# Kernel optimization log

Measured on AMD Instinct MI355X. Metric: run time of the kernel, lower is better.

## Reference

```python
import jax, jax.numpy as jnp
import numpy as np
import math

B, S, D, H = 4, 2048, 1024, 16
HD = D // H  # 64

def setup_inputs() -> dict:
    key = jax.random.key(0)
    ks = jax.random.split(key, 4)
    x = jax.random.normal(ks[0], (B, S, D), dtype=jnp.float32)
    # causal mask, True = attend (precomputed as in the original usage)
    mask = jnp.tril(jnp.ones((S, S), dtype=bool))[None, None, :, :]
    c_attn_w = jax.random.normal(ks[1], (D, 3 * D), dtype=jnp.float32) * 0.02
    c_attn_b = jnp.zeros((3 * D,), dtype=jnp.float32)
    c_proj_w = jax.random.normal(ks[2], (D, D), dtype=jnp.float32) * 0.02
    c_proj_b = jnp.zeros((D,), dtype=jnp.float32)
    return {"x": x, "mask": mask, "c_attn_w": c_attn_w, "c_attn_b": c_attn_b,
            "c_proj_w": c_proj_w, "c_proj_b": c_proj_b}

def reference(x, mask, c_attn_w, c_attn_b, c_proj_w, c_proj_b):
    b, s, d = x.shape
    # c_attn: Conv1D acts as Linear with transposed weight convention
    qkv = x @ c_attn_w + c_attn_b                      # [B,S,3D]
    q, k, v = jnp.split(qkv, 3, axis=-1)
    q = q.reshape(b, s, H, HD).transpose(0, 2, 1, 3)   # [B,H,S,hd]
    k = k.reshape(b, s, H, HD).transpose(0, 2, 1, 3)   # [B,H,S,hd]
    v = v.reshape(b, s, H, HD).transpose(0, 2, 1, 3)   # [B,H,S,hd]
    # scores, scale by sqrt(head_dim) (done unconditionally in _attn)
    w = jnp.einsum('bhqd,bhkd->bhqk', q, k) / math.sqrt(HD)
    # masked_fill_(1 - mask, -10000.0)
    w = jnp.where(mask, w, jnp.float32(-10000.0))
    w = jax.nn.softmax(w, axis=-1)                     # attn_dropout p=0
    a = jnp.einsum('bhqk,bhkd->bhqd', w, v)            # [B,H,S,hd]
    a = a.transpose(0, 2, 1, 3).reshape(b, s, d)       # merge heads
    out = a @ c_proj_w + c_proj_b                      # resid_dropout p=0
    return out
```

## Files before the change

kernel.cpp:

```cpp
#include <hip/hip_runtime.h>

#define SEQ  2048
#define DIM  1024
#define NH   16
#define HD   64
#define NB   4

typedef __bf16 bf16_t;
typedef bf16_t bf16x8 __attribute__((ext_vector_type(8)));
typedef bf16_t bf16x4 __attribute__((ext_vector_type(4)));
typedef float  floatx4 __attribute__((ext_vector_type(4)));

#define MFMA16(a, b, c) __builtin_amdgcn_mfma_f32_16x16x32_bf16((a), (b), (c), 0, 0, 0)

__device__ __forceinline__ void gl_lds16(const bf16_t* g, bf16_t* l) {
    __builtin_amdgcn_global_load_lds(
        (const __attribute__((address_space(1))) void*)g,
        (__attribute__((address_space(3))) void*)l,
        16, 0, 0);
}

__global__ __launch_bounds__(256) void prep(
    const float* __restrict__ x, bf16_t* __restrict__ xb,
    const float* __restrict__ wqkv, bf16_t* __restrict__ wqkvT,
    const float* __restrict__ wproj, bf16_t* __restrict__ wprojT) {
    const int bid = blockIdx.x, tid = threadIdx.x;
    if (bid < 8192) {
        const int i = (bid * 256 + tid) * 4;
        const float4 v = *(const float4*)(x + i);
        xb[i + 0] = (bf16_t)v.x;
        xb[i + 1] = (bf16_t)v.y;
        xb[i + 2] = (bf16_t)v.z;
        xb[i + 3] = (bf16_t)v.w;
        return;
    }
    __shared__ bf16_t t[32][33];
    const float* in;
    bf16_t* out;
    int R, C, bx, by;
    if (bid < 8192 + 3072) {
        const int idx = bid - 8192;
        in = wqkv; out = wqkvT; R = 1024; C = 3072;
        bx = idx % 96; by = idx / 96;
    } else {
        const int idx = bid - 11264;
        in = wproj; out = wprojT; R = 1024; C = 1024;
        bx = idx & 31; by = idx >> 5;
    }
    const int c0 = bx * 32, r0 = by * 32;
    const int tx = tid & 31, ty = tid >> 5;
#pragma unroll
    for (int i = 0; i < 32; i += 8)
        t[ty + i][tx] = (bf16_t)in[(r0 + ty + i) * C + c0 + tx];
    __syncthreads();
#pragma unroll
    for (int i = 0; i < 32; i += 8)
        out[(c0 + ty + i) * R + r0 + tx] = t[tx][ty + i];
}

template <int MODE>
__global__ __launch_bounds__(256, 2) void gemm128(
    const bf16_t* __restrict__ A, const bf16_t* __restrict__ Bt,
    const float* __restrict__ bias, int K,
    bf16_t* __restrict__ Qo, bf16_t* __restrict__ Ko, bf16_t* __restrict__ Vo,
    float* __restrict__ Co) {
    __shared__ __align__(16) bf16_t smem[MODE == 0 ? 128 * 136 : 128 * 128];
    bf16_t* Al = smem;
    bf16_t* Bl = smem + 128 * 64;

    const int tid = threadIdx.x;
    const int m0 = blockIdx.y * 128, n0 = blockIdx.x * 128;
    const int w = tid >> 6, lane = tid & 63;
    const int l15 = lane & 15, quad = lane >> 4;
    const int wm = (w & 1) * 64, wn = (w >> 1) * 64;

    floatx4 acc[4][4] = {};

    const int g_st = ((tid & 7) - (tid >> 3)) & 7;
    const bf16_t* aptr = A + (m0 + (tid >> 3)) * K + g_st * 8;
    const bf16_t* bptr = Bt + (n0 + (tid >> 3)) * K + g_st * 8;
    bf16_t* al = Al + tid * 8;
    bf16_t* bl = Bl + tid * 8;

    for (int k0 = 0; k0 < K; k0 += 64) {
#pragma unroll
        for (int c = 0; c < 4; c++) {
            gl_lds16(aptr + (c * 32) * K, al + c * 2048);
            gl_lds16(bptr + (c * 32) * K, bl + c * 2048);
        }
        aptr += 64;
        bptr += 64;
        __syncthreads();

#pragma unroll
        for (int h = 0; h < 2; h++) {
            const int sAB = (((h << 2) + quad + (l15 & 7)) & 7) * 8;
            bf16x8 af[4], bfr[4];
#pragma unroll
            for (int i = 0; i < 4; i++)
                af[i] = *(const bf16x8*)&Al[(wm + i * 16 + l15) * 64 + sAB];
#pragma unroll
            for (int j = 0; j < 4; j++)
                bfr[j] = *(const bf16x8*)&Bl[(wn + j * 16 + l15) * 64 + sAB];
#pragma unroll
            for (int i = 0; i < 4; i++)
#pragma unroll
                for (int j = 0; j < 4; j++)
                    acc[i][j] = MODE == 0 ? MFMA16(bfr[j], af[i], acc[i][j])
                                          : MFMA16(af[i], bfr[j], acc[i][j]);
        }
        __syncthreads();
    }

    if (MODE == 0) {
        bf16_t* Cl = smem;
        const int which = n0 >> 10;
        const float qs = (which == 0) ? 0.18033688f : 1.0f;
#pragma unroll
        for (int j = 0; j < 4; j++) {
            const int nc = wn + j * 16 + quad * 4;
#pragma unroll
            for (int i = 0; i < 4; i++) {
                const int mrow = wm + i * 16 + l15;
                bf16x4 pk;
#pragma unroll
                for (int r = 0; r < 4; r++)
                    pk[r] = (bf16_t)((acc[i][j][r] + bias[n0 + nc + r]) * qs);
                *(bf16x4*)&Cl[mrow * 136 + nc] = pk;
            }
        }
        __syncthreads();

        if (which < 2) {
            const int row = tid >> 1, ch = (tid & 1) << 6;
            const int m = m0 + row, b = m >> 11, s = m & 2047;
            const int h = ((n0 & 1023) >> 6) + (ch >> 6);
            bf16_t* dst = (which == 0 ? Qo : Ko) + ((size_t)(b * NH + h) * SEQ + s) * HD;
            const bf16_t* src = Cl + row * 136 + ch;
#pragma unroll
            for (int g = 0; g < 8; g++)
                *(bf16x8*)(dst + g * 8) = *(const bf16x8*)(src + g * 8);
        } else {
            const int dl = tid & 127, sh = (tid >> 7) << 6;
            const int h = ((n0 & 1023) >> 6) + (dl >> 6), d = dl & 63;
            const int b = m0 >> 11, sbase = (m0 & 2047) + sh;
            bf16_t* dst = Vo + ((size_t)(b * NH + h) * HD + d) * SEQ + sbase;
#pragma unroll
            for (int g = 0; g < 8; g++) {
                bf16x8 tv;
#pragma unroll
                for (int e = 0; e < 8; e++)
                    tv[e] = Cl[(sh + g * 8 + e) * 136 + dl];
                *(bf16x8*)(dst + g * 8) = tv;
            }
        }
    } else {
#pragma unroll
        for (int j = 0; j < 4; j++) {
            const int n = n0 + wn + j * 16 + l15;
            const float bv = bias[n];
#pragma unroll
            for (int i = 0; i < 4; i++)
#pragma unroll
                for (int r = 0; r < 4; r++) {
                    const int m = m0 + wm + i * 16 + quad * 4 + r;
                    Co[m * 1024 + n] = acc[i][j][r] + bv;
                }
        }
    }
}

__global__ __launch_bounds__(256, 2) void attn2q(
    const bf16_t* __restrict__ Q, const bf16_t* __restrict__ Kg,
    const bf16_t* __restrict__ Vt, bf16_t* __restrict__ Aout) {
    __shared__ __align__(16) bf16_t Ks[2 * 64 * 64];
    __shared__ __align__(16) bf16_t Vs[2 * 64 * 64];
    __shared__ __align__(16) bf16_t Ps[128 * 64];

    const int bh = blockIdx.x;
    const int px = (blockIdx.y + (bh >> 3)) & 7;
    const int qtA = 15 - px, qtB = px;
    const int nkA = 2 * qtA + 2, nkB = 2 * qtB + 2;

    const int tid = threadIdx.x, w = tid >> 6, lane = tid & 63;
    const int l15 = lane & 15, quad = lane >> 4;
    const int b = bh >> 4, hd = bh & 15;
    const int xk = l15 & 7;

    bf16x8 aqA[2][2], aqB[2][2];
#pragma unroll
    for (int i = 0; i < 2; i++) {
        const bf16_t* qrA = Q + (size_t)(bh * SEQ + qtA * 128 + w * 32 + i * 16 + l15) * HD;
        const bf16_t* qrB = Q + (size_t)(bh * SEQ + qtB * 128 + w * 32 + i * 16 + l15) * HD;
#pragma unroll
        for (int h = 0; h < 2; h++) {
            aqA[i][h] = *(const bf16x8*)(qrA + h * 32 + quad * 8);
            aqB[i][h] = *(const bf16x8*)(qrB + h * 32 + quad * 8);
        }
    }

    floatx4 oA[2][4] = {}, oB[2][4] = {};
    float liA[2] = {}, liB[2] = {};

    const int srow = tid >> 3;
    const int sg = (tid & 7) ^ (srow & 7);
    const bf16_t* kgl = Kg + (size_t)bh * SEQ * HD + (size_t)srow * HD + sg * 8;
    const bf16_t* vgl = Vt + (size_t)bh * HD * SEQ + (size_t)srow * SEQ + sg * 8;

    auto stage = [&](int buf, int kt) {
        const bf16_t* kp = kgl + kt * (64 * HD);
        const bf16_t* vp = vgl + kt * 64;
        bf16_t* kd = Ks + buf * 4096 + tid * 8;
        bf16_t* vd = Vs + buf * 4096 + tid * 8;
        gl_lds16(kp, kd);
        gl_lds16(kp + 32 * HD, kd + 2048);
        gl_lds16(vp, vd);
        gl_lds16(vp + 32 * SEQ, vd + 2048);
    };

    auto proc = [&](int qt, bf16x8 (&aq)[2][2], floatx4 (&o)[2][4],
                    float (&li)[2], int kt, int buf) {
        const bf16_t* Ksub = Ks + buf * 4096;
        const bf16_t* Vsub = Vs + buf * 4096;
        bf16x8 bk[4][2];
#pragma unroll
        for (int j = 0; j < 4; j++) {
            const int n = j * 16 + l15;
#pragma unroll
            for (int h = 0; h < 2; h++)
                bk[j][h] = *(const bf16x8*)&Ksub[n * 64 + (((h * 4 + quad) ^ xk) * 8)];
        }
        floatx4 z[2][4] = {};
        __builtin_amdgcn_s_setprio(1);
#pragma unroll
        for (int i = 0; i < 2; i++)
#pragma unroll
            for (int j = 0; j < 4; j++) {
                z[i][j] = MFMA16(bk[j][0], aq[i][0], z[i][j]);
                z[i][j] = MFMA16(bk[j][1], aq[i][1], z[i][j]);
            }
        __builtin_amdgcn_s_setprio(0);
#pragma unroll
        for (int i = 0; i < 2; i++) {
            const int qbase = qt * 128 + w * 32 + i * 16;
            const int qrow_l = qbase + l15;
            const bool full = (kt * 64 + 63) <= qbase;
            const int prow = w * 32 + i * 16 + l15;
            bf16_t* pbase = Ps + prow * 64;
            const int rx = prow & 7;
#pragma unroll
            for (int j = 0; j < 4; j++) {
                const int kg0 = kt * 64 + j * 16 + quad * 4;
                bf16x4 pk;
                float es[4];
#pragma unroll
                for (int r = 0; r < 4; r++) {
                    float e = __builtin_amdgcn_exp2f(z[i][j][r]);
                    if (!full && kg0 + r > qrow_l) e = 0.f;
                    es[r] = e;
                    pk[r] = (bf16_t)e;
                }
                li[i] += (es[0] + es[1]) + (es[2] + es[3]);
                const int g = 2 * j + (quad >> 1);
                *(bf16x4*)(pbase + (((g ^ rx) << 3) | ((quad & 1) << 2))) = pk;
            }
        }
        __builtin_amdgcn_s_waitcnt(0xC07F);
        bf16x8 ap[2][2];
#pragma unroll
        for (int i = 0; i < 2; i++) {
            const int row = w * 32 + i * 16 + l15;
#pragma unroll
            for (int kk = 0; kk < 2; kk++)
                ap[i][kk] = *(const bf16x8*)&Ps[row * 64 +
                                               (((kk * 4 + quad) ^ (row & 7)) << 3)];
        }
        bf16x8 bv[4][2];
#pragma unroll
        for (int j = 0; j < 4; j++) {
            const int n = j * 16 + l15;
#pragma unroll
            for (int kk = 0; kk < 2; kk++)
                bv[j][kk] = *(const bf16x8*)&Vsub[n * 64 + (((kk * 4 + quad) ^ xk) * 8)];
        }
        __builtin_amdgcn_s_setprio(1);
#pragma unroll
        for (int i = 0; i < 2; i++)
#pragma unroll
            for (int j = 0; j < 4; j++) {
                o[i][j] = MFMA16(ap[i][0], bv[j][0], o[i][j]);
                o[i][j] = MFMA16(ap[i][1], bv[j][1], o[i][j]);
            }
        __builtin_amdgcn_s_setprio(0);
    };

    stage(0, 0);
    __syncthreads();
    for (int kt = 0; kt < nkA; ++kt) {
        const int cur = kt & 1;
        if (kt + 1 < nkA) stage(cur ^ 1, kt + 1);
        proc(qtA, aqA, oA, liA, kt, cur);
        if (kt < nkB) proc(qtB, aqB, oB, liB, kt, cur);
        __syncthreads();
    }

#pragma unroll
    for (int t = 0; t < 2; t++) {
        const int qt = t == 0 ? qtA : qtB;
        floatx4(&o)[2][4] = t == 0 ? oA : oB;
        float(&li)[2] = t == 0 ? liA : liB;
#pragma unroll
        for (int i = 0; i < 2; i++) {
            float s = li[i];
            s += __shfl_xor(s, 16, 64);
            s += __shfl_xor(s, 32, 64);
#pragma unroll
            for (int r = 0; r < 4; r++) {
                const float sv = __shfl(s, quad * 4 + r, 64);
                const float inv = 1.0f / sv;
                const int srow_o = qt * 128 + w * 32 + i * 16 + quad * 4 + r;
                bf16_t* orow = Aout + (size_t)(b * SEQ + srow_o) * DIM + hd * HD;
#pragma unroll
                for (int j = 0; j < 4; j++)
                    orow[j * 16 + l15] = (bf16_t)(o[i][j][r] * inv);
            }
        }
    }
}

extern "C" void kernel_launch(void* const* d_in, const int* in_sizes, int n_in,
                              void* d_out, int out_size, void* d_ws, size_t ws_size,
                              hipStream_t stream) {
    const float* x        = (const float*)d_in[0];
    const float* c_attn_w = (const float*)d_in[2];
    const float* c_attn_b = (const float*)d_in[3];
    const float* c_proj_w = (const float*)d_in[4];
    const float* c_proj_b = (const float*)d_in[5];
    float* out = (float*)d_out;

    char* ws = (char*)d_ws;
    bf16_t* xb     = (bf16_t*)ws; ws += (size_t)NB * SEQ * DIM * 2;
    bf16_t* wqkvT  = (bf16_t*)ws; ws += (size_t)3072 * 1024 * 2;
    bf16_t* wprojT = (bf16_t*)ws; ws += (size_t)1024 * 1024 * 2;
    bf16_t* Qb  = (bf16_t*)ws; ws += (size_t)NB * NH * SEQ * HD * 2;
    bf16_t* Kb  = (bf16_t*)ws; ws += (size_t)NB * NH * SEQ * HD * 2;
    bf16_t* Vtb = (bf16_t*)ws; ws += (size_t)NB * SEQ * DIM * 2 / 16;
    bf16_t* Ab  = (bf16_t*)ws; ws += (size_t)NB * SEQ * DIM * 2;

    prep<<<12288, 256, 0, stream>>>(x, xb, c_attn_w, wqkvT, c_proj_w, wprojT);

    gemm128<0><<<dim3(24, 64), 256, 0, stream>>>(xb, wqkvT, c_attn_b, 1024,
                                                 Qb, Kb, Vtb, nullptr);

    attn2q<<<dim3(NB * NH, 8), 256, 0, stream>>>(Qb, Kb, Vtb, Ab);

    gemm128<1><<<dim3(8, 64), 256, 0, stream>>>(Ab, wprojT, c_proj_b, 1024,
                                                nullptr, nullptr, nullptr, out);
}
```

Measured before the change: 252.2 us.

## Split paired-query-tile attention blocks into one tile per block with higher occupancy

The attention kernel used to pair a long and a short causal query tile in each block so that work per block stayed balanced. Each block now handles a single 128-row query tile, the grid grows from 8 to 16 tiles per head, and launch bounds request 3 blocks per CU instead of 2. This trades the balanced pairing and the shared K/V staging between two tiles for more parallelism and fewer live registers. It also fixes the workspace size of the V-transpose buffer, which was too small before.

Measured after the change: 260.0 us. +3.1%, slower.

```diff
diff --git a/kernel.cpp b/kernel.cpp
--- a/kernel.cpp
+++ b/kernel.cpp
@@ -170,7 +170,7 @@
     }
 }
 
-__global__ __launch_bounds__(256, 2) void attn2q(
+__global__ __launch_bounds__(256, 3) void attn1q(
     const bf16_t* __restrict__ Q, const bf16_t* __restrict__ Kg,
     const bf16_t* __restrict__ Vt, bf16_t* __restrict__ Aout) {
     __shared__ __align__(16) bf16_t Ks[2 * 64 * 64];
@@ -178,29 +178,25 @@
     __shared__ __align__(16) bf16_t Ps[128 * 64];
 
     const int bh = blockIdx.x;
-    const int px = (blockIdx.y + (bh >> 3)) & 7;
-    const int qtA = 15 - px, qtB = px;
-    const int nkA = 2 * qtA + 2, nkB = 2 * qtB + 2;
+    const int qt = 15 - blockIdx.y;
+    const int nk = 2 * qt + 2;
 
     const int tid = threadIdx.x, w = tid >> 6, lane = tid & 63;
     const int l15 = lane & 15, quad = lane >> 4;
     const int b = bh >> 4, hd = bh & 15;
     const int xk = l15 & 7;
 
-    bf16x8 aqA[2][2], aqB[2][2];
+    bf16x8 aq[2][2];
 #pragma unroll
     for (int i = 0; i < 2; i++) {
-        const bf16_t* qrA = Q + (size_t)(bh * SEQ + qtA * 128 + w * 32 + i * 16 + l15) * HD;
-        const bf16_t* qrB = Q + (size_t)(bh * SEQ + qtB * 128 + w * 32 + i * 16 + l15) * HD;
-#pragma unroll
-        for (int h = 0; h < 2; h++) {
-            aqA[i][h] = *(const bf16x8*)(qrA + h * 32 + quad * 8);
-            aqB[i][h] = *(const bf16x8*)(qrB + h * 32 + quad * 8);
-        }
-    }
-
-    floatx4 oA[2][4] = {}, oB[2][4] = {};
-    float liA[2] = {}, liB[2] = {};
+        const bf16_t* qr = Q + (size_t)(bh * SEQ + qt * 128 + w * 32 + i * 16 + l15) * HD;
+#pragma unroll
+        for (int h = 0; h < 2; h++)
+            aq[i][h] = *(const bf16x8*)(qr + h * 32 + quad * 8);
+    }
+
+    floatx4 o[2][4] = {};
+    float li[2] = {};
 
     const int srow = tid >> 3;
     const int sg = (tid & 7) ^ (srow & 7);
@@ -218,8 +214,7 @@
         gl_lds16(vp + 32 * SEQ, vd + 2048);
     };
 
-    auto proc = [&](int qt, bf16x8 (&aq)[2][2], floatx4 (&o)[2][4],
-                    float (&li)[2], int kt, int buf) {
+    auto proc = [&](int kt, int buf) {
         const bf16_t* Ksub = Ks + buf * 4096;
         const bf16_t* Vsub = Vs + buf * 4096;
         bf16x8 bk[4][2];
@@ -296,34 +291,27 @@
 
     stage(0, 0);
     __syncthreads();
-    for (int kt = 0; kt < nkA; ++kt) {
+    for (int kt = 0; kt < nk; ++kt) {
         const int cur = kt & 1;
-        if (kt + 1 < nkA) stage(cur ^ 1, kt + 1);
-        proc(qtA, aqA, oA, liA, kt, cur);
-        if (kt < nkB) proc(qtB, aqB, oB, liB, kt, cur);
+        if (kt + 1 < nk) stage(cur ^ 1, kt + 1);
+        proc(kt, cur);
         __syncthreads();
     }
 
 #pragma unroll
-    for (int t = 0; t < 2; t++) {
-        const int qt = t == 0 ? qtA : qtB;
-        floatx4(&o)[2][4] = t == 0 ? oA : oB;
-        float(&li)[2] = t == 0 ? liA : liB;
-#pragma unroll
-        for (int i = 0; i < 2; i++) {
-            float s = li[i];
-            s += __shfl_xor(s, 16, 64);
-            s += __shfl_xor(s, 32, 64);
-#pragma unroll
-            for (int r = 0; r < 4; r++) {
-                const float sv = __shfl(s, quad * 4 + r, 64);
-                const float inv = 1.0f / sv;
-                const int srow_o = qt * 128 + w * 32 + i * 16 + quad * 4 + r;
-                bf16_t* orow = Aout + (size_t)(b * SEQ + srow_o) * DIM + hd * HD;
-#pragma unroll
-                for (int j = 0; j < 4; j++)
-                    orow[j * 16 + l15] = (bf16_t)(o[i][j][r] * inv);
-            }
+    for (int i = 0; i < 2; i++) {
+        float s = li[i];
+        s += __shfl_xor(s, 16, 64);
+        s += __shfl_xor(s, 32, 64);
+#pragma unroll
+        for (int r = 0; r < 4; r++) {
+            const float sv = __shfl(s, quad * 4 + r, 64);
+            const float inv = 1.0f / sv;
+            const int srow_o = qt * 128 + w * 32 + i * 16 + quad * 4 + r;
+            bf16_t* orow = Aout + (size_t)(b * SEQ + srow_o) * DIM + hd * HD;
+#pragma unroll
+            for (int j = 0; j < 4; j++)
+                orow[j * 16 + l15] = (bf16_t)(o[i][j][r] * inv);
         }
     }
 }
@@ -344,7 +332,7 @@
     bf16_t* wprojT = (bf16_t*)ws; ws += (size_t)1024 * 1024 * 2;
     bf16_t* Qb  = (bf16_t*)ws; ws += (size_t)NB * NH * SEQ * HD * 2;
     bf16_t* Kb  = (bf16_t*)ws; ws += (size_t)NB * NH * SEQ * HD * 2;
-    bf16_t* Vtb = (bf16_t*)ws; ws += (size_t)NB * SEQ * DIM * 2 / 16;
+    bf16_t* Vtb = (bf16_t*)ws; ws += (size_t)NB * NH * SEQ * HD * 2;
     bf16_t* Ab  = (bf16_t*)ws; ws += (size_t)NB * SEQ * DIM * 2;
 
     prep<<<12288, 256, 0, stream>>>(x, xb, c_attn_w, wqkvT, c_proj_w, wprojT);
@@ -352,7 +340,7 @@
     gemm128<0><<<dim3(24, 64), 256, 0, stream>>>(xb, wqkvT, c_attn_b, 1024,
                                                  Qb, Kb, Vtb, nullptr);
 
-    attn2q<<<dim3(NB * NH, 8), 256, 0, stream>>>(Qb, Kb, Vtb, Ab);
+    attn1q<<<dim3(NB * NH, 16), 256, 0, stream>>>(Qb, Kb, Vtb, Ab);
 
     gemm128<1><<<dim3(8, 64), 256, 0, stream>>>(Ab, wprojT, c_proj_b, 1024,
                                                 nullptr, nullptr, nullptr, out);
```
